# Performance work log

Measured on AMD Instinct MI355X. Metric: run time of the kernel, lower is better.

Reference implementation:

```python
import jax, jax.numpy as jnp
import numpy as np
import math

D_MODEL = 1024
NUM_HEADS = 16
D_K = D_MODEL // NUM_HEADS
B, NQ, NK = 2, 2048, 2048


def setup_inputs() -> dict:
    key = jax.random.key(0)
    ks = jax.random.split(key, 14)
    s = 1.0 / math.sqrt(D_MODEL)
    inp = {
        "query": jax.random.normal(ks[0], (B, NQ, D_MODEL), jnp.float32),
        "key": jax.random.normal(ks[1], (B, NK, D_MODEL), jnp.float32),
        "value": jax.random.normal(ks[2], (B, NK, D_MODEL), jnp.float32),
        "mask": jax.random.randint(ks[3], (B, NK), 0, 2, jnp.int32),
        "attn_bias": jax.random.normal(ks[4], (B, NQ, NK), jnp.float32),
        "w_q": jax.random.normal(ks[5], (D_MODEL, D_MODEL), jnp.float32) * s,
        "b_q": jnp.zeros((D_MODEL,), jnp.float32),
        "w_k": jax.random.normal(ks[6], (D_MODEL, D_MODEL), jnp.float32) * s,
        "b_k": jnp.zeros((D_MODEL,), jnp.float32),
        "w_v": jax.random.normal(ks[7], (D_MODEL, D_MODEL), jnp.float32) * s,
        "b_v": jnp.zeros((D_MODEL,), jnp.float32),
        "w_o": jax.random.normal(ks[8], (D_MODEL, D_MODEL), jnp.float32) * s,
        "b_o": jnp.zeros((D_MODEL,), jnp.float32),
    }
    return inp


def reference(query, key, value, mask, attn_bias, w_q, b_q, w_k, b_k, w_v, b_v, w_o, b_o):
    # Linear projections (torch Linear: x @ W^T + b), reshape to [B, H, N, d_k]
    def proj(x, w, b, n):
        return (x @ w.T + b).reshape(x.shape[0], n, NUM_HEADS, D_K).transpose(0, 2, 1, 3)

    Q = proj(query, w_q, b_q, query.shape[1])   # [B,H,Nq,dk]
    K = proj(key, w_k, b_k, key.shape[1])       # [B,H,Nk,dk]
    V = proj(value, w_v, b_v, value.shape[1])   # [B,H,Nk,dk]

    scores = jnp.einsum("bhqd,bhkd->bhqk", Q, K) / math.sqrt(D_K)
    scores = scores + attn_bias[:, None, :, :]           # bias broadcast over heads
    pad = (mask[:, None, None, :] == 0)                   # [B,1,1,Nk]
    scores = jnp.where(pad, jnp.float32(-1e9), scores)
    attn = jax.nn.softmax(scores, axis=-1)                # dropout is identity (eval)
    out = jnp.einsum("bhqk,bhkd->bhqd", attn, V)          # [B,H,Nq,dk]
    out = out.transpose(0, 2, 1, 3).reshape(query.shape[0], query.shape[1], D_MODEL)
    return out @ w_o.T + b_o
```

## Files before the change

### kernel.cpp

```cpp
#include <hip/hip_runtime.h>
#include <hip/hip_bf16.h>


typedef short bf16x8 __attribute__((ext_vector_type(8)));
typedef short bf16x4 __attribute__((ext_vector_type(4)));
typedef float f32x4 __attribute__((ext_vector_type(4)));
typedef float f32x16 __attribute__((ext_vector_type(16)));
typedef int i32x4 __attribute__((ext_vector_type(4)));
typedef unsigned short u16;
typedef unsigned short u16x8 __attribute__((ext_vector_type(8)));
typedef unsigned short u16x4 __attribute__((ext_vector_type(4)));

#define MFMA16(a, b, c) __builtin_amdgcn_mfma_f32_16x16x32_bf16((a), (b), (c), 0, 0, 0)
#define MFMA32(a, b, c) __builtin_amdgcn_mfma_f32_32x32x16_bf16((a), (b), (c), 0, 0, 0)
#define GLD16(gp, lp)                                                     \
  __builtin_amdgcn_global_load_lds(                                       \
      (const __attribute__((address_space(1))) void*)(gp),                \
      (__attribute__((address_space(3))) void*)(lp), 16, 0, 0)

#define WAITVM_BAR(N) asm volatile("s_waitcnt vmcnt(" #N ")\ns_barrier" ::: "memory")
#define BAR() asm volatile("s_barrier" ::: "memory")

#if __has_builtin(__builtin_amdgcn_exp2f)
#define EXP2(x) __builtin_amdgcn_exp2f(x)
#else
#define EXP2(x) exp2f(x)
#endif

__device__ __forceinline__ u16 f2bf(float f) {
  union { float f; unsigned u; } v; v.f = f;
  return (u16)((v.u + 0x7fffu + ((v.u >> 16) & 1u)) >> 16);
}
__device__ __forceinline__ unsigned pkc(float lo, float hi) {
  __hip_bfloat162 h = __float22bfloat162_rn(float2{lo, hi});
  union { __hip_bfloat162 h; unsigned u; } c; c.h = h;
  return c.u;
}
__device__ __forceinline__ void pl32swap(unsigned& a, unsigned& b) {
  asm("v_permlane32_swap_b32 %0, %1" : "+v"(a), "+v"(b));
}

struct ConvDesc { const float* src; u16* dst; int n; };
struct ConvArgs { ConvDesc d[7]; };

__device__ __forceinline__ void biasprep_body(const float* __restrict__ bias,
                                              const int* __restrict__ mask,
                                              u16* __restrict__ out, int i) {
  const int o0 = i * 16;
  const int rowg = o0 >> 11;
  const int b = rowg >> 11;
  const int off = o0 & 2047;
  const int c = off >> 5;
  const int hi = (off >> 4) & 1;
  const float* src = bias + (size_t)rowg * 2048 + c * 32 + hi * 4;
  const int* msk = mask + b * 2048 + c * 32 + hi * 4;
  u16x8 w0 = {}, w1 = {};
#pragma unroll
  for (int t = 0; t < 4; t++) {
    f32x4 v = *(const f32x4*)(src + t * 8);
    i32x4 m = *(const i32x4*)(msk + t * 8);
#pragma unroll
    for (int j = 0; j < 4; j++) {
      u16 val = (m[j] != 0) ? f2bf(v[j] * 1.44269504f) : (u16)0xFF80;
      if (t < 2) w0[t * 4 + j] = val;
      else       w1[(t - 2) * 4 + j] = val;
    }
  }
  *(u16x8*)(out + o0) = w0;
  *(u16x8*)(out + o0 + 8) = w1;
}

__global__ __launch_bounds__(256)
void k_prep(ConvArgs a, const float* __restrict__ bias,
            const int* __restrict__ mask, u16* __restrict__ bout) {
  if (blockIdx.y == 7) {
    biasprep_body(bias, mask, bout, blockIdx.x * 256 + threadIdx.x);
    return;
  }
  ConvDesc cd = a.d[blockIdx.y];
  int i = (blockIdx.x * 256 + threadIdx.x) * 8;
  if (i >= cd.n) return;
  const float4* s = (const float4*)(cd.src + i);
  float4 f0 = s[0], f1 = s[1];
  u16x8 o;
  o[0] = f2bf(f0.x); o[1] = f2bf(f0.y); o[2] = f2bf(f0.z); o[3] = f2bf(f0.w);
  o[4] = f2bf(f1.x); o[5] = f2bf(f1.y); o[6] = f2bf(f1.z); o[7] = f2bf(f1.w);
  *(u16x8*)(cd.dst + i) = o;
}

__global__ __launch_bounds__(256)
void k_biasprep(const float* __restrict__ bias, const int* __restrict__ mask,
                u16* __restrict__ out) {
  biasprep_body(bias, mask, out, blockIdx.x * 256 + threadIdx.x);
}

template <int MF>
__device__ __forceinline__ void gemm_impl(const u16* __restrict__ A,
                                          const u16* __restrict__ Bw,
                                          const float* __restrict__ bias,
                                          void* __restrict__ outp, int mode,
                                          float oscale) {
  __shared__ u16 As[2][MF * 1024];
  __shared__ u16 Bs[2][4096];
  const int tid = threadIdx.x;
  const int lane = tid & 63;
  const int wv = tid >> 6;
  const int wr = wv >> 1, wc = wv & 1;
  const int m0 = blockIdx.y * (MF * 32), n0 = blockIdx.x * 128;

  f32x4 acc[MF][4] = {};

  const int s0 = tid, s1 = 256 + tid;
  const int r0 = s0 >> 2, c0 = (s0 & 3) ^ (r0 & 3);
  const int r1 = s1 >> 2, c1 = (s1 & 3) ^ (r1 & 3);
  const u16* gA0 = A + (size_t)(m0 + r0) * 1024 + c0 * 8;
  const u16* gA1 = A + (size_t)(m0 + r1) * 1024 + c1 * 8;
  const u16* gB0 = Bw + (size_t)(n0 + r0) * 1024 + c0 * 8;
  const u16* gB1 = Bw + (size_t)(n0 + r1) * 1024 + c1 * 8;
  u16* lA0 = &As[0][(tid & ~63) * 8];
  u16* lB0 = &Bs[0][(tid & ~63) * 8];

  GLD16(gA0, lA0);
  if constexpr (MF == 4) GLD16(gA1, lA0 + 2048);
  GLD16(gB0, lB0);
  GLD16(gB1, lB0 + 2048);
  WAITVM_BAR(0);

#define GSTEP(BUF, K0)                                                     \
  {                                                                        \
    const int nk = ((K0) + 32) & 1023;                                     \
    GLD16(gA0 + nk, lA0 + ((BUF) ^ 1) * (MF * 1024));                      \
    if constexpr (MF == 4)                                                 \
      GLD16(gA1 + nk, lA0 + 2048 + ((BUF) ^ 1) * (MF * 1024));             \
    GLD16(gB0 + nk, lB0 + ((BUF) ^ 1) * 4096);                             \
    GLD16(gB1 + nk, lB0 + 2048 + ((BUF) ^ 1) * 4096);                      \
    if constexpr (MF == 4) { WAITVM_BAR(4); } else { WAITVM_BAR(3); }      \
    bf16x8 af[MF], bfr[4];                                                 \
    _Pragma("unroll")                                                      \
    for (int mi = 0; mi < MF; mi++) {                                      \
      int row = wr * (MF * 16) + mi * 16 + (lane & 15);                    \
      int byt = row * 64 + (((lane >> 4) * 16) ^ ((row & 3) << 4));        \
      af[mi] = *(const bf16x8*)((const char*)&As[BUF][0] + byt);           \
    }                                                                      \
    _Pragma("unroll")                                                      \
    for (int ni = 0; ni < 4; ni++) {                                       \
      int row = wc * 64 + ni * 16 + (lane & 15);                           \
      int byt = row * 64 + (((lane >> 4) * 16) ^ ((row & 3) << 4));        \
      bfr[ni] = *(const bf16x8*)((const char*)&Bs[BUF][0] + byt);          \
    }                                                                      \
    __builtin_amdgcn_s_setprio(1);                                         \
    _Pragma("unroll")                                                      \
    for (int mi = 0; mi < MF; mi++)                                        \
      _Pragma("unroll")                                                    \
      for (int ni = 0; ni < 4; ni++)                                       \
        acc[mi][ni] = MFMA16(af[mi], bfr[ni], acc[mi][ni]);                \
    __builtin_amdgcn_s_setprio(0);                                         \
    BAR();                                                                 \
  }

  for (int k0 = 0; k0 < 1024; k0 += 64) {
    GSTEP(0, k0)
    GSTEP(1, k0 + 32)
  }
#undef GSTEP

#pragma unroll
  for (int ni = 0; ni < 4; ni++) {
    int n = n0 + wc * 64 + ni * 16 + (lane & 15);
    float bv = bias[n];
#pragma unroll
    for (int mi = 0; mi < MF; mi++) {
      int mb = m0 + wr * (MF * 16) + mi * 16 + (lane >> 4) * 4;
      if (mode == 2) {
        float* O = (float*)outp;
#pragma unroll
        for (int r = 0; r < 4; r++)
          O[(size_t)(mb + r) * 1024 + n] = (acc[mi][ni][r] + bv) * oscale;
      } else if (mode == 0) {
        u16* O = (u16*)outp;
        int b = mb >> 11, q = mb & 2047;
        int h = n >> 6, dk = n & 63;
        size_t base = ((size_t)(b * 16 + h) * 2048 + q) * 64 + dk;
#pragma unroll
        for (int r = 0; r < 4; r++)
          O[base + (size_t)r * 64] = f2bf((acc[mi][ni][r] + bv) * oscale);
      } else {
        u16* O = (u16*)outp;
        int b = mb >> 11, kv = mb & 2047;
        int h = n >> 6, dk = n & 63;
        u16x4 pk;
#pragma unroll
        for (int r = 0; r < 4; r++) pk[r] = f2bf((acc[mi][ni][r] + bv) * oscale);
        *(u16x4*)((u16*)O + ((size_t)((b * 16 + h) * 64 + dk)) * 2048 + kv) = pk;
      }
    }
  }
}

struct GemmDesc { const u16* A; const u16* W; const float* bias; void* out;
                  int mode; float oscale; };
struct Gemm3 { GemmDesc d[3]; };

__global__ __launch_bounds__(256, 3) void k_gemm_qkv(Gemm3 g3) {
  GemmDesc gd = g3.d[blockIdx.z];
  gemm_impl<4>(gd.A, gd.W, gd.bias, gd.out, gd.mode, gd.oscale);
}
__global__ __launch_bounds__(256, 2)
void k_gemm_o(const u16* __restrict__ A, const u16* __restrict__ W,
              const float* __restrict__ bias, float* __restrict__ out) {
  gemm_impl<2>(A, W, bias, out, 2, 1.0f);
}

__global__ __launch_bounds__(256, 2)
void k_attn(const u16* __restrict__ Qb, const u16* __restrict__ Kb,
            const u16* __restrict__ Vt, const u16* __restrict__ BiasE,
            u16* __restrict__ Ob) {
  __shared__ u16 Ks[2][128 * 64];
  __shared__ u16 Vs[2][64 * 128];

  const int tid = threadIdx.x, lane = tid & 63, w = tid >> 6;
  const int l31 = lane & 31, hi2 = lane >> 5;
  const int bid = blockIdx.x;
  const int xcd = bid & 7, rr = bid >> 3;
  const int qt = rr & 15;
  const int pr = xcd + 8 * (rr >> 4);
  const int b = pr >> 4, h = pr & 15;
  const int q0 = qt * 128;
  const size_t bh = (size_t)(b * 16 + h);

  const u16* Qrow = Qb + (bh * 2048 + q0 + w * 32 + l31) * 64 + hi2 * 8;
  bf16x8 bq[4];
#pragma unroll
  for (int dc = 0; dc < 4; dc++) bq[dc] = *(const bf16x8*)(Qrow + dc * 16);

  f32x16 acc[2] = {};
  float lrun = 0.f;

  const u16* Kg = Kb + bh * 2048 * 64;
  const u16* Vg = Vt + bh * 64 * 2048;
  int rK[4], cK[4], rV[4], cV[4], ldd[4];
#pragma unroll
  for (int i = 0; i < 4; i++) {
    int s = i * 256 + tid;
    rK[i] = s >> 3; cK[i] = (s & 7) ^ (rK[i] & 7);
    rV[i] = s >> 4; cV[i] = (s & 15) ^ (rV[i] & 7);
    ldd[i] = (i * 256 + (tid & ~63)) * 8;
  }
  const int kx = (lane & 7) << 4;

  const u16* brow =
      BiasE + ((size_t)b * 2048 + q0 + w * 32 + l31) * 2048 + hi2 * 16;

#pragma unroll
  for (int i = 0; i < 4; i++)
    GLD16(Kg + (size_t)rK[i] * 64 + cK[i] * 8, &Ks[0][ldd[i]]);
#pragma unroll
  for (int i = 0; i < 4; i++)
    GLD16(Vg + (size_t)rV[i] * 2048 + cV[i] * 8, &Vs[0][ldd[i]]);
  u16x8 bb[4][2];
#pragma unroll
  for (int c = 0; c < 4; c++) {
    bb[c][0] = *(const u16x8*)(brow + c * 32);
    bb[c][1] = *(const u16x8*)(brow + c * 32 + 8);
  }

#define ATTN_STEP(BUF, T)                                                      \
  {                                                                            \
    WAITVM_BAR(0);            \
    const char* kb = (const char*)&Ks[BUF][0];                                 \
    const char* vb = (const char*)&Vs[BUF][0];                                 \
    f32x16 sc[4];                                                              \
    __builtin_amdgcn_s_setprio(1);                                             \
    _Pragma("unroll")                                                          \
    for (int c = 0; c < 4; c++) {                                              \
      f32x16 z;                                                                \
      _Pragma("unroll")                                                        \
      for (int r = 0; r < 8; r++)                                              \
        z[r] = __uint_as_float((unsigned)bb[c][0][r] << 16);                   \
      _Pragma("unroll")                                                        \
      for (int r = 0; r < 8; r++)                                              \
        z[8 + r] = __uint_as_float((unsigned)bb[c][1][r] << 16);               \
      const int rowb = (c * 32 + l31) * 128;                                   \
      _Pragma("unroll")                                                        \
      for (int dc = 0; dc < 4; dc++) {                                         \
        bf16x8 ak =                                                            \
            *(const bf16x8*)(kb + rowb + ((dc * 32 + hi2 * 16) ^ kx));         \
        z = MFMA32(ak, bq[dc], z);                                             \
      }                                                                        \
      sc[c] = z;                                                               \
    }                                                                          \
    __builtin_amdgcn_s_setprio(0);                                             \
    const int nkv = (((T) + 1) & 15) * 128;                                    \
    _Pragma("unroll")                                                          \
    for (int i = 0; i < 4; i++)                                                \
      GLD16(Kg + (size_t)(nkv + rK[i]) * 64 + cK[i] * 8,                       \
            &Ks[(BUF) ^ 1][ldd[i]]);                                           \
    _Pragma("unroll")                                                          \
    for (int i = 0; i < 4; i++)                                                \
      GLD16(Vg + (size_t)rV[i] * 2048 + nkv + cV[i] * 8,                       \
            &Vs[(BUF) ^ 1][ldd[i]]);                                           \
    _Pragma("unroll")                                                          \
    for (int c = 0; c < 4; c++) {                                              \
      bb[c][0] = *(const u16x8*)(brow + nkv + c * 32);                         \
      bb[c][1] = *(const u16x8*)(brow + nkv + c * 32 + 8);                     \
    }                                                                          \
     \
    _Pragma("unroll")                                                          \
    for (int c = 0; c < 4; c++)                                                \
      _Pragma("unroll")                                                        \
      for (int r = 0; r < 16; r++) sc[c][r] = EXP2(sc[c][r]);                  \
    float cs[4];                                                               \
    _Pragma("unroll")                                                          \
    for (int c = 0; c < 4; c++) {                                              \
      float s8[8];                                                             \
      _Pragma("unroll")                                                        \
      for (int r = 0; r < 8; r++) s8[r] = sc[c][r] + sc[c][r + 8];             \
      float s4[4];                                                             \
      _Pragma("unroll")                                                        \
      for (int r = 0; r < 4; r++) s4[r] = s8[r] + s8[r + 4];                   \
      cs[c] = (s4[0] + s4[1]) + (s4[2] + s4[3]);                               \
    }                                                                          \
    lrun += (cs[0] + cs[1]) + (cs[2] + cs[3]);                                 \
    __builtin_amdgcn_s_setprio(1);                                             \
    _Pragma("unroll")                                                          \
    for (int c = 0; c < 4; c++) {                                              \
      unsigned a0 = pkc(sc[c][0], sc[c][1]), b0 = pkc(sc[c][4], sc[c][5]);     \
      unsigned a1 = pkc(sc[c][2], sc[c][3]), b1 = pkc(sc[c][6], sc[c][7]);     \
      unsigned e0 = pkc(sc[c][8], sc[c][9]), f0 = pkc(sc[c][12], sc[c][13]);   \
      unsigned e1 = pkc(sc[c][10], sc[c][11]), f1 = pkc(sc[c][14], sc[c][15]); \
      pl32swap(a0, b0); pl32swap(a1, b1);                                      \
      pl32swap(e0, f0); pl32swap(e1, f1);                                      \
      union { unsigned u[4]; bf16x8 v; } fe, fo;                               \
      fe.u[0] = a0; fe.u[1] = a1; fe.u[2] = b0; fe.u[3] = b1;                  \
      fo.u[0] = e0; fo.u[1] = e1; fo.u[2] = f0; fo.u[3] = f1;                  \
      _Pragma("unroll")                                                        \
      for (int ds = 0; ds < 2; ds++) {                                         \
        const int vrow = (ds * 32 + l31) * 256;                                \
        bf16x8 ve =                                                            \
            *(const bf16x8*)(vb + vrow + (((c * 4 + hi2) * 16) ^ kx));         \
        acc[ds] = MFMA32(ve, fe.v, acc[ds]);                                   \
        bf16x8 vo =                                                            \
            *(const bf16x8*)(vb + vrow + (((c * 4 + 2 + hi2) * 16) ^ kx));     \
        acc[ds] = MFMA32(vo, fo.v, acc[ds]);                                   \
      }                                                                        \
    }                                                                          \
    __builtin_amdgcn_s_setprio(0);                                             \
  }

  for (int t = 0; t < 16; t += 2) {
    ATTN_STEP(0, t)
    ATTN_STEP(1, t + 1)
  }
#undef ATTN_STEP

  lrun += __shfl_xor(lrun, 32, 64);
  float linv = 1.0f / lrun;
  const size_t obase =
      ((size_t)b * 2048 + q0 + w * 32 + l31) * 1024 + h * 64 + hi2 * 4;
#pragma unroll
  for (int ds = 0; ds < 2; ds++)
#pragma unroll
    for (int t = 0; t < 4; t++) {
      u16x4 pk;
#pragma unroll
      for (int j = 0; j < 4; j++) pk[j] = f2bf(acc[ds][t * 4 + j] * linv);
      *(u16x4*)(Ob + obase + ds * 32 + t * 8) = pk;
    }
}

extern "C" void kernel_launch(void* const* d_in, const int* in_sizes, int n_in,
                              void* d_out, int out_size, void* d_ws,
                              size_t ws_size, hipStream_t stream) {
  (void)in_sizes; (void)n_in; (void)out_size;
  const float* q_in = (const float*)d_in[0];
  const float* k_in = (const float*)d_in[1];
  const float* v_in = (const float*)d_in[2];
  const int* mask = (const int*)d_in[3];
  const float* attn_bias = (const float*)d_in[4];
  const float* w_q = (const float*)d_in[5];
  const float* b_q = (const float*)d_in[6];
  const float* w_k = (const float*)d_in[7];
  const float* b_k = (const float*)d_in[8];
  const float* w_v = (const float*)d_in[9];
  const float* b_v = (const float*)d_in[10];
  const float* w_o = (const float*)d_in[11];
  const float* b_o = (const float*)d_in[12];

  const size_t MB = 1u << 20;
  char* ws = (char*)d_ws;
  u16* XQ = (u16*)(ws + 0 * MB);
  u16* XK = (u16*)(ws + 8 * MB);
  u16* XV = (u16*)(ws + 16 * MB);
  u16* WQ = (u16*)(ws + 24 * MB);
  u16* WK = (u16*)(ws + 26 * MB);
  u16* WV = (u16*)(ws + 28 * MB);
  u16* WO = (u16*)(ws + 30 * MB);
  u16* Qb = (u16*)(ws + 32 * MB);
  u16* Kb = (u16*)(ws + 40 * MB);
  u16* Vt = (u16*)(ws + 48 * MB);
  u16* Ob = (u16*)(ws + 56 * MB);
  const bool merged = ws_size >= (size_t)80 * MB;
  u16* BiasE = (u16*)(ws + (merged ? 64 : 0) * MB);

  ConvArgs ca;
  ca.d[0] = {q_in, XQ, 4096 * 1024};
  ca.d[1] = {k_in, XK, 4096 * 1024};
  ca.d[2] = {v_in, XV, 4096 * 1024};
  ca.d[3] = {w_q, WQ, 1024 * 1024};
  ca.d[4] = {w_k, WK, 1024 * 1024};
  ca.d[5] = {w_v, WV, 1024 * 1024};
  ca.d[6] = {w_o, WO, 1024 * 1024};
  k_prep<<<dim3(2048, merged ? 8 : 7), 256, 0, stream>>>(ca, attn_bias, mask,
                                                         BiasE);

  const float QSCALE = 0.125f * 1.44269504f;
  Gemm3 g3;
  g3.d[0] = {XQ, WQ, b_q, (void*)Qb, 0, QSCALE};
  g3.d[1] = {XK, WK, b_k, (void*)Kb, 0, 1.0f};
  g3.d[2] = {XV, WV, b_v, (void*)Vt, 1, 1.0f};
  k_gemm_qkv<<<dim3(8, 32, 3), 256, 0, stream>>>(g3);

  if (!merged) k_biasprep<<<2048, 256, 0, stream>>>(attn_bias, mask, BiasE);

  k_attn<<<512, 256, 0, stream>>>(Qb, Kb, Vt, BiasE, Ob);

  k_gemm_o<<<dim3(8, 64), 256, 0, stream>>>(Ob, WO, b_o, (float*)d_out);
}
```

Before: 141.6 us.

## Split attention KV range across two wave groups per block with LDS reduction

The attention kernel now launches 512 threads per block. Each half processes half of the key/value sequence (1024 keys) in 64-key tiles, with its own double-buffered LDS region. At the end, the second half writes its partial accumulators and row sums to LDS, and the first half combines them, normalizes and writes the output. This doubles the waves per block to raise latency hiding on the 512-block grid, at the cost of a cross-wave reduction and smaller tiles per step.

```diff
diff --git a/kernel.cpp b/kernel.cpp
--- a/kernel.cpp
+++ b/kernel.cpp
@@ -211,15 +211,15 @@
   gemm_impl<2>(A, W, bias, out, 2, 1.0f);
 }
 
-__global__ __launch_bounds__(256, 2)
+__global__ __launch_bounds__(512, 4)
 void k_attn(const u16* __restrict__ Qb, const u16* __restrict__ Kb,
             const u16* __restrict__ Vt, const u16* __restrict__ BiasE,
             u16* __restrict__ Ob) {
-  __shared__ u16 Ks[2][128 * 64];
-  __shared__ u16 Vs[2][64 * 128];
+  __shared__ __attribute__((aligned(16))) char LB[65536];
 
   const int tid = threadIdx.x, lane = tid & 63, w = tid >> 6;
   const int l31 = lane & 31, hi2 = lane >> 5;
+  const int qg = w & 3, sp = w >> 2;
   const int bid = blockIdx.x;
   const int xcd = bid & 7, rr = bid >> 3;
   const int qt = rr & 15;
@@ -227,8 +227,11 @@
   const int b = pr >> 4, h = pr & 15;
   const int q0 = qt * 128;
   const size_t bh = (size_t)(b * 16 + h);
-
-  const u16* Qrow = Qb + (bh * 2048 + q0 + w * 32 + l31) * 64 + hi2 * 8;
+  const int kvb = sp * 1024;
+
+  char* spb = LB + sp * 32768;
+
+  const u16* Qrow = Qb + (bh * 2048 + q0 + qg * 32 + l31) * 64 + hi2 * 8;
   bf16x8 bq[4];
 #pragma unroll
   for (int dc = 0; dc < 4; dc++) bq[dc] = *(const bf16x8*)(Qrow + dc * 16);
@@ -238,41 +241,38 @@
 
   const u16* Kg = Kb + bh * 2048 * 64;
   const u16* Vg = Vt + bh * 64 * 2048;
-  int rK[4], cK[4], rV[4], cV[4], ldd[4];
-#pragma unroll
-  for (int i = 0; i < 4; i++) {
-    int s = i * 256 + tid;
-    rK[i] = s >> 3; cK[i] = (s & 7) ^ (rK[i] & 7);
-    rV[i] = s >> 4; cV[i] = (s & 15) ^ (rV[i] & 7);
-    ldd[i] = (i * 256 + (tid & ~63)) * 8;
-  }
+
+  const int ts = qg * 64 + lane;
+  const int sA = ts, sB = ts + 256;
+  const int rA = sA >> 3, cA = (sA & 7) ^ (rA & 7);
+  const int rB = sB >> 3, cB = (sB & 7) ^ (rB & 7);
+  const int ld0 = (ts & ~63) * 16;
+  const int ld1 = ld0 + 4096;
   const int kx = (lane & 7) << 4;
 
   const u16* brow =
-      BiasE + ((size_t)b * 2048 + q0 + w * 32 + l31) * 2048 + hi2 * 16;
-
-#pragma unroll
-  for (int i = 0; i < 4; i++)
-    GLD16(Kg + (size_t)rK[i] * 64 + cK[i] * 8, &Ks[0][ldd[i]]);
-#pragma unroll
-  for (int i = 0; i < 4; i++)
-    GLD16(Vg + (size_t)rV[i] * 2048 + cV[i] * 8, &Vs[0][ldd[i]]);
-  u16x8 bb[4][2];
-#pragma unroll
-  for (int c = 0; c < 4; c++) {
-    bb[c][0] = *(const u16x8*)(brow + c * 32);
-    bb[c][1] = *(const u16x8*)(brow + c * 32 + 8);
-  }
-
-#define ATTN_STEP(BUF, T)                                                      \
+      BiasE + ((size_t)b * 2048 + q0 + qg * 32 + l31) * 2048 + hi2 * 16;
+
+  GLD16(Kg + (size_t)(kvb + rA) * 64 + cA * 8, spb + ld0);
+  GLD16(Kg + (size_t)(kvb + rB) * 64 + cB * 8, spb + ld1);
+  GLD16(Vg + (size_t)rA * 2048 + kvb + cA * 8, spb + 16384 + ld0);
+  GLD16(Vg + (size_t)rB * 2048 + kvb + cB * 8, spb + 16384 + ld1);
+  u16x8 bb[2][2];
+#pragma unroll
+  for (int c = 0; c < 2; c++) {
+    bb[c][0] = *(const u16x8*)(brow + kvb + c * 32);
+    bb[c][1] = *(const u16x8*)(brow + kvb + c * 32 + 8);
+  }
+
+#define ATTN_STEP(BUF, T, STAGE)                                               \
   {                                                                            \
     WAITVM_BAR(0);            \
-    const char* kb = (const char*)&Ks[BUF][0];                                 \
-    const char* vb = (const char*)&Vs[BUF][0];                                 \
-    f32x16 sc[4];                                                              \
+    const char* kb = spb + (BUF) * 8192;                                       \
+    const char* vb = spb + 16384 + (BUF) * 8192;                               \
+    f32x16 sc[2];                                                              \
     __builtin_amdgcn_s_setprio(1);                                             \
     _Pragma("unroll")                                                          \
-    for (int c = 0; c < 4; c++) {                                              \
+    for (int c = 0; c < 2; c++) {                                              \
       f32x16 z;                                                                \
       _Pragma("unroll")                                                        \
       for (int r = 0; r < 8; r++)                                              \
@@ -290,28 +290,30 @@
       sc[c] = z;                                                               \
     }                                                                          \
     __builtin_amdgcn_s_setprio(0);                                             \
-    const int nkv = (((T) + 1) & 15) * 128;                                    \
-    _Pragma("unroll")                                                          \
-    for (int i = 0; i < 4; i++)                                                \
-      GLD16(Kg + (size_t)(nkv + rK[i]) * 64 + cK[i] * 8,                       \
-            &Ks[(BUF) ^ 1][ldd[i]]);                                           \
-    _Pragma("unroll")                                                          \
-    for (int i = 0; i < 4; i++)                                                \
-      GLD16(Vg + (size_t)rV[i] * 2048 + nkv + cV[i] * 8,                       \
-            &Vs[(BUF) ^ 1][ldd[i]]);                                           \
-    _Pragma("unroll")                                                          \
-    for (int c = 0; c < 4; c++) {                                              \
-      bb[c][0] = *(const u16x8*)(brow + nkv + c * 32);                         \
-      bb[c][1] = *(const u16x8*)(brow + nkv + c * 32 + 8);                     \
+    if (STAGE) {                                                               \
+      const int nkv = kvb + ((T) + 1) * 64;                                    \
+      GLD16(Kg + (size_t)(nkv + rA) * 64 + cA * 8,                             \
+            spb + ((BUF) ^ 1) * 8192 + ld0);                                   \
+      GLD16(Kg + (size_t)(nkv + rB) * 64 + cB * 8,                             \
+            spb + ((BUF) ^ 1) * 8192 + ld1);                                   \
+      GLD16(Vg + (size_t)rA * 2048 + nkv + cA * 8,                             \
+            spb + 16384 + ((BUF) ^ 1) * 8192 + ld0);                           \
+      GLD16(Vg + (size_t)rB * 2048 + nkv + cB * 8,                             \
+            spb + 16384 + ((BUF) ^ 1) * 8192 + ld1);                           \
+      _Pragma("unroll")                                                        \
+      for (int c = 0; c < 2; c++) {                                            \
+        bb[c][0] = *(const u16x8*)(brow + nkv + c * 32);                       \
+        bb[c][1] = *(const u16x8*)(brow + nkv + c * 32 + 8);                   \
+      }                                                                        \
     }                                                                          \
      \
     _Pragma("unroll")                                                          \
-    for (int c = 0; c < 4; c++)                                                \
+    for (int c = 0; c < 2; c++)                                                \
       _Pragma("unroll")                                                        \
       for (int r = 0; r < 16; r++) sc[c][r] = EXP2(sc[c][r]);                  \
-    float cs[4];                                                               \
+    float cs[2];                                                               \
     _Pragma("unroll")                                                          \
-    for (int c = 0; c < 4; c++) {                                              \
+    for (int c = 0; c < 2; c++) {                                              \
       float s8[8];                                                             \
       _Pragma("unroll")                                                        \
       for (int r = 0; r < 8; r++) s8[r] = sc[c][r] + sc[c][r + 8];             \
@@ -320,10 +322,10 @@
       for (int r = 0; r < 4; r++) s4[r] = s8[r] + s8[r + 4];                   \
       cs[c] = (s4[0] + s4[1]) + (s4[2] + s4[3]);                               \
     }                                                                          \
-    lrun += (cs[0] + cs[1]) + (cs[2] + cs[3]);                                 \
+    lrun += cs[0] + cs[1];                                                     \
     __builtin_amdgcn_s_setprio(1);                                             \
     _Pragma("unroll")                                                          \
-    for (int c = 0; c < 4; c++) {                                              \
+    for (int c = 0; c < 2; c++) {                                              \
       unsigned a0 = pkc(sc[c][0], sc[c][1]), b0 = pkc(sc[c][4], sc[c][5]);     \
       unsigned a1 = pkc(sc[c][2], sc[c][3]), b1 = pkc(sc[c][6], sc[c][7]);     \
       unsigned e0 = pkc(sc[c][8], sc[c][9]), f0 = pkc(sc[c][12], sc[c][13]);   \
@@ -335,7 +337,7 @@
       fo.u[0] = e0; fo.u[1] = e1; fo.u[2] = f0; fo.u[3] = f1;                  \
       _Pragma("unroll")                                                        \
       for (int ds = 0; ds < 2; ds++) {                                         \
-        const int vrow = (ds * 32 + l31) * 256;                                \
+        const int vrow = (ds * 32 + l31) * 128;                                \
         bf16x8 ve =                                                            \
             *(const bf16x8*)(vb + vrow + (((c * 4 + hi2) * 16) ^ kx));         \
         acc[ds] = MFMA32(ve, fe.v, acc[ds]);                                   \
@@ -347,25 +349,47 @@
     __builtin_amdgcn_s_setprio(0);                                             \
   }
 
-  for (int t = 0; t < 16; t += 2) {
-    ATTN_STEP(0, t)
-    ATTN_STEP(1, t + 1)
-  }
+  for (int t = 0; t < 14; t += 2) {
+    ATTN_STEP(0, t, 1)
+    ATTN_STEP(1, t + 1, 1)
+  }
+  ATTN_STEP(0, 14, 1)
+  ATTN_STEP(1, 15, 0)
 #undef ATTN_STEP
 
-  lrun += __shfl_xor(lrun, 32, 64);
-  float linv = 1.0f / lrun;
-  const size_t obase =
-      ((size_t)b * 2048 + q0 + w * 32 + l31) * 1024 + h * 64 + hi2 * 4;
-#pragma unroll
-  for (int ds = 0; ds < 2; ds++)
-#pragma unroll
-    for (int t = 0; t < 4; t++) {
-      u16x4 pk;
-#pragma unroll
-      for (int j = 0; j < 4; j++) pk[j] = f2bf(acc[ds][t * 4 + j] * linv);
-      *(u16x4*)(Ob + obase + ds * 32 + t * 8) = pk;
-    }
+  __syncthreads();
+  char* cb = LB + qg * 8448;
+  if (sp == 1) {
+#pragma unroll
+    for (int ds = 0; ds < 2; ds++)
+#pragma unroll
+      for (int r4 = 0; r4 < 4; r4++) {
+        float4 v = make_float4(acc[ds][r4 * 4 + 0], acc[ds][r4 * 4 + 1],
+                               acc[ds][r4 * 4 + 2], acc[ds][r4 * 4 + 3]);
+        *(float4*)(cb + ds * 4096 + r4 * 1024 + lane * 16) = v;
+      }
+    *(float*)(cb + 8192 + lane * 4) = lrun;
+  }
+  __syncthreads();
+  if (sp == 0) {
+    lrun += *(const float*)(cb + 8192 + lane * 4);
+    lrun += __shfl_xor(lrun, 32, 64);
+    float linv = 1.0f / lrun;
+    const size_t obase =
+        ((size_t)b * 2048 + q0 + qg * 32 + l31) * 1024 + h * 64 + hi2 * 4;
+#pragma unroll
+    for (int ds = 0; ds < 2; ds++)
+#pragma unroll
+      for (int t = 0; t < 4; t++) {
+        float4 p1 = *(const float4*)(cb + ds * 4096 + t * 1024 + lane * 16);
+        u16x4 pk;
+        pk[0] = f2bf((acc[ds][t * 4 + 0] + p1.x) * linv);
+        pk[1] = f2bf((acc[ds][t * 4 + 1] + p1.y) * linv);
+        pk[2] = f2bf((acc[ds][t * 4 + 2] + p1.z) * linv);
+        pk[3] = f2bf((acc[ds][t * 4 + 3] + p1.w) * linv);
+        *(u16x4*)(Ob + obase + ds * 32 + t * 8) = pk;
+      }
+  }
 }
 
 extern "C" void kernel_launch(void* const* d_in, const int* in_sizes, int n_in,
@@ -422,7 +446,7 @@
 
   if (!merged) k_biasprep<<<2048, 256, 0, stream>>>(attn_bias, mask, BiasE);
 
-  k_attn<<<512, 256, 0, stream>>>(Qb, Kb, Vt, BiasE, Ob);
+  k_attn<<<512, 512, 0, stream>>>(Qb, Kb, Vt, BiasE, Ob);
 
   k_gemm_o<<<dim3(8, 64), 256, 0, stream>>>(Ob, WO, b_o, (float*)d_out);
 }
```

Result: slower. 187.7 us (+32.6%).

## Fuse fp32-to-bf16 activation conversion into QKV GEMM operand loads

Applied to the files above, without the earlier changes.

The QKV projection GEMM now reads the fp32 query/key/value activations directly, converts them to bf16 in registers, and stores them into shared memory. The separate conversion pass in the prep kernel, which wrote bf16 copies of the inputs to workspace, is removed, and the fallback bias-prep kernel path is dropped. This removes a full write and re-read of the three activation tensors. The cost is twice the global read bytes per A tile, a register-staged path instead of direct global-to-LDS loads, and extra conversion ALU work and an LDS wait inside the GEMM loop. Each A row is also reloaded by every N-tile block.

```diff
diff --git a/kernel.cpp b/kernel.cpp
--- a/kernel.cpp
+++ b/kernel.cpp
@@ -20,6 +20,9 @@
 
 #define WAITVM_BAR(N) asm volatile("s_waitcnt vmcnt(" #N ")\ns_barrier" ::: "memory")
 #define BAR() asm volatile("s_barrier" ::: "memory")
+#define LGKM_BAR() asm volatile("s_waitcnt lgkmcnt(0)\ns_barrier" ::: "memory")
+#define WAITALL_BAR() \
+  asm volatile("s_waitcnt vmcnt(0) lgkmcnt(0)\ns_barrier" ::: "memory")
 
 #if __has_builtin(__builtin_amdgcn_exp2f)
 #define EXP2(x) __builtin_amdgcn_exp2f(x)
@@ -41,7 +44,7 @@
 }
 
 struct ConvDesc { const float* src; u16* dst; int n; };
-struct ConvArgs { ConvDesc d[7]; };
+struct ConvArgs { ConvDesc d[4]; };
 
 __device__ __forceinline__ void biasprep_body(const float* __restrict__ bias,
                                               const int* __restrict__ mask,
@@ -73,7 +76,7 @@
 __global__ __launch_bounds__(256)
 void k_prep(ConvArgs a, const float* __restrict__ bias,
             const int* __restrict__ mask, u16* __restrict__ bout) {
-  if (blockIdx.y == 7) {
+  if (blockIdx.y == 4) {
     biasprep_body(bias, mask, bout, blockIdx.x * 256 + threadIdx.x);
     return;
   }
@@ -88,14 +91,8 @@
   *(u16x8*)(cd.dst + i) = o;
 }
 
-__global__ __launch_bounds__(256)
-void k_biasprep(const float* __restrict__ bias, const int* __restrict__ mask,
-                u16* __restrict__ out) {
-  biasprep_body(bias, mask, out, blockIdx.x * 256 + threadIdx.x);
-}
-
-template <int MF>
-__device__ __forceinline__ void gemm_impl(const u16* __restrict__ A,
+template <int MF, bool AF32>
+__device__ __forceinline__ void gemm_impl(const void* __restrict__ Ap,
                                           const u16* __restrict__ Bw,
                                           const float* __restrict__ bias,
                                           void* __restrict__ outp, int mode,
@@ -108,33 +105,60 @@
   const int wr = wv >> 1, wc = wv & 1;
   const int m0 = blockIdx.y * (MF * 32), n0 = blockIdx.x * 128;
 
+  const u16* A16 = (const u16*)Ap;
+  const float* A32 = (const float*)Ap;
+
   f32x4 acc[MF][4] = {};
 
   const int s0 = tid, s1 = 256 + tid;
   const int r0 = s0 >> 2, c0 = (s0 & 3) ^ (r0 & 3);
   const int r1 = s1 >> 2, c1 = (s1 & 3) ^ (r1 & 3);
-  const u16* gA0 = A + (size_t)(m0 + r0) * 1024 + c0 * 8;
-  const u16* gA1 = A + (size_t)(m0 + r1) * 1024 + c1 * 8;
+  const u16* gA0 = A16 + (size_t)(m0 + r0) * 1024 + c0 * 8;
+  const u16* gA1 = A16 + (size_t)(m0 + r1) * 1024 + c1 * 8;
+  const float* fA0 = A32 + (size_t)(m0 + r0) * 1024 + c0 * 8;
+  const float* fA1 = A32 + (size_t)(m0 + r1) * 1024 + c1 * 8;
   const u16* gB0 = Bw + (size_t)(n0 + r0) * 1024 + c0 * 8;
   const u16* gB1 = Bw + (size_t)(n0 + r1) * 1024 + c1 * 8;
   u16* lA0 = &As[0][(tid & ~63) * 8];
   u16* lB0 = &Bs[0][(tid & ~63) * 8];
 
-  GLD16(gA0, lA0);
-  if constexpr (MF == 4) GLD16(gA1, lA0 + 2048);
+  if constexpr (AF32) {
+    f32x4 a0 = *(const f32x4*)(fA0), a1 = *(const f32x4*)(fA0 + 4);
+    f32x4 a2 = *(const f32x4*)(fA1), a3 = *(const f32x4*)(fA1 + 4);
+    union { unsigned u[4]; bf16x8 v; } w0, w1;
+    w0.u[0] = pkc(a0[0], a0[1]); w0.u[1] = pkc(a0[2], a0[3]);
+    w0.u[2] = pkc(a1[0], a1[1]); w0.u[3] = pkc(a1[2], a1[3]);
+    w1.u[0] = pkc(a2[0], a2[1]); w1.u[1] = pkc(a2[2], a2[3]);
+    w1.u[2] = pkc(a3[0], a3[1]); w1.u[3] = pkc(a3[2], a3[3]);
+    *(bf16x8*)((char*)&As[0][0] + tid * 16) = w0.v;
+    *(bf16x8*)((char*)&As[0][0] + (256 + tid) * 16) = w1.v;
+  } else {
+    GLD16(gA0, lA0);
+    if constexpr (MF == 4) GLD16(gA1, lA0 + 2048);
+  }
   GLD16(gB0, lB0);
   GLD16(gB1, lB0 + 2048);
-  WAITVM_BAR(0);
+  WAITALL_BAR();
 
 #define GSTEP(BUF, K0)                                                     \
   {                                                                        \
     const int nk = ((K0) + 32) & 1023;                                     \
-    GLD16(gA0 + nk, lA0 + ((BUF) ^ 1) * (MF * 1024));                      \
-    if constexpr (MF == 4)                                                 \
-      GLD16(gA1 + nk, lA0 + 2048 + ((BUF) ^ 1) * (MF * 1024));             \
+    f32x4 av0, av1, av2, av3;                                              \
+    if constexpr (AF32) {   \
+      av0 = *(const f32x4*)(fA0 + nk);                                     \
+      av1 = *(const f32x4*)(fA0 + nk + 4);                                 \
+      av2 = *(const f32x4*)(fA1 + nk);                                     \
+      av3 = *(const f32x4*)(fA1 + nk + 4);                                 \
+    } else {                                                               \
+      GLD16(gA0 + nk, lA0 + ((BUF) ^ 1) * (MF * 1024));                    \
+      if constexpr (MF == 4)                                               \
+        GLD16(gA1 + nk, lA0 + 2048 + ((BUF) ^ 1) * (MF * 1024));           \
+    }                                                                      \
     GLD16(gB0 + nk, lB0 + ((BUF) ^ 1) * 4096);                             \
     GLD16(gB1 + nk, lB0 + 2048 + ((BUF) ^ 1) * 4096);                      \
-    if constexpr (MF == 4) { WAITVM_BAR(4); } else { WAITVM_BAR(3); }      \
+    if constexpr (AF32) { WAITVM_BAR(6); }                                 \
+    else if constexpr (MF == 4) { WAITVM_BAR(4); }                         \
+    else { WAITVM_BAR(3); }                                                \
     bf16x8 af[MF], bfr[4];                                                 \
     _Pragma("unroll")                                                      \
     for (int mi = 0; mi < MF; mi++) {                                      \
@@ -155,7 +179,18 @@
       for (int ni = 0; ni < 4; ni++)                                       \
         acc[mi][ni] = MFMA16(af[mi], bfr[ni], acc[mi][ni]);                \
     __builtin_amdgcn_s_setprio(0);                                         \
-    BAR();                                                                 \
+    if constexpr (AF32) {               \
+      union { unsigned u[4]; bf16x8 v; } w0, w1;                           \
+      w0.u[0] = pkc(av0[0], av0[1]); w0.u[1] = pkc(av0[2], av0[3]);        \
+      w0.u[2] = pkc(av1[0], av1[1]); w0.u[3] = pkc(av1[2], av1[3]);        \
+      w1.u[0] = pkc(av2[0], av2[1]); w1.u[1] = pkc(av2[2], av2[3]);        \
+      w1.u[2] = pkc(av3[0], av3[1]); w1.u[3] = pkc(av3[2], av3[3]);        \
+      *(bf16x8*)((char*)&As[(BUF) ^ 1][0] + tid * 16) = w0.v;              \
+      *(bf16x8*)((char*)&As[(BUF) ^ 1][0] + (256 + tid) * 16) = w1.v;      \
+      LGKM_BAR();   \
+    } else {                                                               \
+      BAR();                                                               \
+    }                                                                      \
   }
 
   for (int k0 = 0; k0 < 1024; k0 += 64) {
@@ -197,18 +232,18 @@
   }
 }
 
-struct GemmDesc { const u16* A; const u16* W; const float* bias; void* out;
+struct GemmDesc { const void* A; const u16* W; const float* bias; void* out;
                   int mode; float oscale; };
 struct Gemm3 { GemmDesc d[3]; };
 
 __global__ __launch_bounds__(256, 3) void k_gemm_qkv(Gemm3 g3) {
   GemmDesc gd = g3.d[blockIdx.z];
-  gemm_impl<4>(gd.A, gd.W, gd.bias, gd.out, gd.mode, gd.oscale);
+  gemm_impl<4, true>(gd.A, gd.W, gd.bias, gd.out, gd.mode, gd.oscale);
 }
 __global__ __launch_bounds__(256, 2)
 void k_gemm_o(const u16* __restrict__ A, const u16* __restrict__ W,
               const float* __restrict__ bias, float* __restrict__ out) {
-  gemm_impl<2>(A, W, bias, out, 2, 1.0f);
+  gemm_impl<2, false>(A, W, bias, out, 2, 1.0f);
 }
 
 __global__ __launch_bounds__(256, 2)
@@ -266,7 +301,7 @@
 
 #define ATTN_STEP(BUF, T)                                                      \
   {                                                                            \
-    WAITVM_BAR(0);            \
+    WAITVM_BAR(0);                                                             \
     const char* kb = (const char*)&Ks[BUF][0];                                 \
     const char* vb = (const char*)&Vs[BUF][0];                                 \
     f32x16 sc[4];                                                              \
@@ -304,7 +339,6 @@
       bb[c][0] = *(const u16x8*)(brow + nkv + c * 32);                         \
       bb[c][1] = *(const u16x8*)(brow + nkv + c * 32 + 8);                     \
     }                                                                          \
-     \
     _Pragma("unroll")                                                          \
     for (int c = 0; c < 4; c++)                                                \
       _Pragma("unroll")                                                        \
@@ -371,7 +405,7 @@
 extern "C" void kernel_launch(void* const* d_in, const int* in_sizes, int n_in,
                               void* d_out, int out_size, void* d_ws,
                               size_t ws_size, hipStream_t stream) {
-  (void)in_sizes; (void)n_in; (void)out_size;
+  (void)in_sizes; (void)n_in; (void)out_size; (void)ws_size;
   const float* q_in = (const float*)d_in[0];
   const float* k_in = (const float*)d_in[1];
   const float* v_in = (const float*)d_in[2];
@@ -388,9 +422,7 @@
 
   const size_t MB = 1u << 20;
   char* ws = (char*)d_ws;
-  u16* XQ = (u16*)(ws + 0 * MB);
-  u16* XK = (u16*)(ws + 8 * MB);
-  u16* XV = (u16*)(ws + 16 * MB);
+  u16* BiasE = (u16*)(ws + 0 * MB);
   u16* WQ = (u16*)(ws + 24 * MB);
   u16* WK = (u16*)(ws + 26 * MB);
   u16* WV = (u16*)(ws + 28 * MB);
@@ -399,29 +431,21 @@
   u16* Kb = (u16*)(ws + 40 * MB);
   u16* Vt = (u16*)(ws + 48 * MB);
   u16* Ob = (u16*)(ws + 56 * MB);
-  const bool merged = ws_size >= (size_t)80 * MB;
-  u16* BiasE = (u16*)(ws + (merged ? 64 : 0) * MB);
 
   ConvArgs ca;
-  ca.d[0] = {q_in, XQ, 4096 * 1024};
-  ca.d[1] = {k_in, XK, 4096 * 1024};
-  ca.d[2] = {v_in, XV, 4096 * 1024};
-  ca.d[3] = {w_q, WQ, 1024 * 1024};
-  ca.d[4] = {w_k, WK, 1024 * 1024};
-  ca.d[5] = {w_v, WV, 1024 * 1024};
-  ca.d[6] = {w_o, WO, 1024 * 1024};
-  k_prep<<<dim3(2048, merged ? 8 : 7), 256, 0, stream>>>(ca, attn_bias, mask,
-                                                         BiasE);
+  ca.d[0] = {w_q, WQ, 1024 * 1024};
+  ca.d[1] = {w_k, WK, 1024 * 1024};
+  ca.d[2] = {w_v, WV, 1024 * 1024};
+  ca.d[3] = {w_o, WO, 1024 * 1024};
+  k_prep<<<dim3(2048, 5), 256, 0, stream>>>(ca, attn_bias, mask, BiasE);
 
   const float QSCALE = 0.125f * 1.44269504f;
   Gemm3 g3;
-  g3.d[0] = {XQ, WQ, b_q, (void*)Qb, 0, QSCALE};
-  g3.d[1] = {XK, WK, b_k, (void*)Kb, 0, 1.0f};
-  g3.d[2] = {XV, WV, b_v, (void*)Vt, 1, 1.0f};
+  g3.d[0] = {q_in, WQ, b_q, (void*)Qb, 0, QSCALE};
+  g3.d[1] = {k_in, WK, b_k, (void*)Kb, 0, 1.0f};
+  g3.d[2] = {v_in, WV, b_v, (void*)Vt, 1, 1.0f};
   k_gemm_qkv<<<dim3(8, 32, 3), 256, 0, stream>>>(g3);
 
-  if (!merged) k_biasprep<<<2048, 256, 0, stream>>>(attn_bias, mask, BiasE);
-
   k_attn<<<512, 256, 0, stream>>>(Qb, Kb, Vt, BiasE, Ob);
 
   k_gemm_o<<<dim3(8, 64), 256, 0, stream>>>(Ob, WO, b_o, (float*)d_out);
```

Result: slower. 159.0 us (+12.3%).
